# Optimization experiments

Measured on AMD Instinct MI355X. Metric: run time of the kernel, lower is better.

## Reference

```python
import jax, jax.numpy as jnp
import numpy as np

D_MODEL = 1024
HEADS = 16
D_K = 64
B, S = 2, 2048


def setup_inputs() -> dict:
    key = jax.random.key(0)
    ks = jax.random.split(key, 12)
    s = 0.02
    return {
        "query": jax.random.normal(ks[0], (B, S, D_MODEL), dtype=jnp.float32),
        "key": jax.random.normal(ks[1], (B, S, D_MODEL), dtype=jnp.float32),
        "value": jax.random.normal(ks[2], (B, S, D_MODEL), dtype=jnp.float32),
        "Wq": jax.random.normal(ks[3], (D_MODEL, HEADS * D_K), dtype=jnp.float32) * s,
        "bq": jnp.zeros((HEADS * D_K,), dtype=jnp.float32),
        "Wk": jax.random.normal(ks[4], (D_MODEL, HEADS * D_K), dtype=jnp.float32) * s,
        "bk": jnp.zeros((HEADS * D_K,), dtype=jnp.float32),
        "Wv": jax.random.normal(ks[5], (D_MODEL, HEADS * D_K), dtype=jnp.float32) * s,
        "bv": jnp.zeros((HEADS * D_K,), dtype=jnp.float32),
        "Wo": jax.random.normal(ks[6], (HEADS * D_K, D_MODEL), dtype=jnp.float32) * s,
        "bo": jnp.zeros((D_MODEL,), dtype=jnp.float32),
    }


def reference(query, key, value, Wq, bq, Wk, bk, Wv, bv, Wo, bo):
    b, s, _ = query.shape
    scale = 1.0 / np.sqrt(D_K).astype(np.float32)
    # project and split heads: [b, s, h, d_k]
    q = (query @ Wq + bq).reshape(b, s, HEADS, D_K)
    k = (key @ Wk + bk).reshape(b, s, HEADS, D_K)
    v = (value @ Wv + bv).reshape(b, s, HEADS, D_K)
    # attention scores [b, i, j, h]
    scores = jnp.einsum('bihd,bjhd->bijh', q, k) * scale
    # NOTE: original uses nn.Softmax(dim=1) -> normalize over query axis i (faithful quirk)
    attn = jax.nn.softmax(scores, axis=1)
    # dropout is identity in eval mode
    x = jnp.einsum('bijh,bjhd->bihd', attn, v).reshape(b, s, HEADS * D_K)
    return x @ Wo + bo
```

## Files before the change

### kernel.cpp

```cpp
#include <hip/hip_runtime.h>
#include <hip/hip_bf16.h>

#define SEQ   2048
#define NH    16
#define DK    64
#define DM    1024
#define NTOK  4096
#define C1    0.1803368801111204f

typedef unsigned short u16;
typedef unsigned int   u32;
typedef short bhalf8 __attribute__((ext_vector_type(8)));
typedef short bhalf4 __attribute__((ext_vector_type(4)));
typedef float floatx4 __attribute__((ext_vector_type(4)));

#define MFMA16(a,b,c) __builtin_amdgcn_mfma_f32_16x16x32_bf16(a,b,c,0,0,0)
#define MFMA4(a,b,c)  __builtin_amdgcn_mfma_f32_16x16x16bf16_1k(a,b,c,0,0,0)

#if __has_builtin(__builtin_amdgcn_exp2f)
#define EXP2(x) __builtin_amdgcn_exp2f(x)
#else
#define EXP2(x) exp2f(x)
#endif

__device__ __forceinline__ u16 f2b(float f){
  union { float f; u32 u; } v; v.f = f;
  u32 r = v.u + 0x7fffu + ((v.u >> 16) & 1u);
  return (u16)(r >> 16);
}
__device__ __forceinline__ u32 pk2(float a, float b){
  union { __hip_bfloat162 h; u32 w; } o;
  o.h = __float22bfloat162_rn(make_float2(a, b));
  return o.w;
}
__device__ __forceinline__ void gld_lds16(const u16* g, u16* lds){
  __builtin_amdgcn_global_load_lds(
      (const __attribute__((address_space(1))) u32*)g,
      (__attribute__((address_space(3))) u32*)lds, 16, 0, 0);
}

__global__ __launch_bounds__(256)
void cvt_qkv(const float* __restrict__ q, const float* __restrict__ k,
             const float* __restrict__ v, u16* __restrict__ Aq,
             u16* __restrict__ Ak, u16* __restrict__ Av)
{
  const float* in = (blockIdx.y == 0) ? q : (blockIdx.y == 1) ? k : v;
  u16* out       = (blockIdx.y == 0) ? Aq : (blockIdx.y == 1) ? Ak : Av;
  const size_t i = ((size_t)blockIdx.x * 256 + threadIdx.x) * 8;
  const float4 a = *(const float4*)(in + i);
  const float4 b = *(const float4*)(in + i + 4);
  uint4 o;
  o.x = pk2(a.x, a.y); o.y = pk2(a.z, a.w);
  o.z = pk2(b.x, b.y); o.w = pk2(b.z, b.w);
  *(uint4*)(out + i) = o;
}

__global__ __launch_bounds__(256)
void wtrans4(const float* __restrict__ Wq, const float* __restrict__ Wk,
             const float* __restrict__ Wv, const float* __restrict__ Wo,
             u16* __restrict__ Wtall)
{
  __shared__ __align__(16) u16 T[64][68];
  const int z = blockIdx.z;
  const float* W = (z == 0) ? Wq : (z == 1) ? Wk : (z == 2) ? Wv : Wo;
  u16* Wt = Wtall + (size_t)z * DM * DM;
  const int k0 = blockIdx.y * 64, n0 = blockIdx.x * 64;
  const int t = threadIdx.x;
  #pragma unroll
  for (int p = 0; p < 16; ++p){
    int e = p*256 + t, k = e >> 6, n = e & 63;
    T[n][k] = f2b(W[(size_t)(k0+k)*DM + n0 + n]);
  }
  __syncthreads();
  #pragma unroll
  for (int p = 0; p < 8; ++p){
    int e = p*256 + t, n = e >> 5, kp = e & 31;
    u32 val = *(const u32*)&T[n][2*kp];
    *(u32*)&Wt[(size_t)(n0+n)*DM + k0 + 2*kp] = val;
  }
}

__global__ __launch_bounds__(256)
void gemm_qkv(const u16* __restrict__ Aq, const u16* __restrict__ Ak,
              const u16* __restrict__ Av, const u16* __restrict__ Wtall,
              const float* __restrict__ bq, const float* __restrict__ bk,
              const float* __restrict__ bv, u16* __restrict__ Qb,
              u16* __restrict__ Kb, u16* __restrict__ Vt)
{
  __shared__ __align__(16) u16 Asm[2][128*32];
  __shared__ __align__(16) u16 Bsm[2][128*32];
  const int z = blockIdx.z;
  const u16* A = (z == 0) ? Aq : (z == 1) ? Ak : Av;
  const u16* Wt = Wtall + (size_t)z * DM * DM;
  const float* bias = (z == 0) ? bq : (z == 1) ? bk : bv;
  const float cmul = (z == 0) ? C1 : 1.0f;

  const int bm = blockIdx.y * 128, bn = blockIdx.x * 128;
  const int t = threadIdx.x, wid = t >> 6, l = t & 63, r16 = l & 15, q = l >> 4;
  const int wm = (wid & 1) * 64, wn = (wid >> 1) * 64;
  const int rL = t >> 2, gL = ((t & 3) ^ (rL & 3)) * 8;
  const u16* Ag = A  + (size_t)(bm + rL)*DM + gL;
  const u16* Bg = Wt + (size_t)(bn + rL)*DM + gL;
  const int wo = wid*512;
  const int sw = (r16 & 3);
  floatx4 acc[4][4] = {};

  gld_lds16(Ag,                  Asm[0] + wo);
  gld_lds16(Ag + (size_t)64*DM,  Asm[0] + wo + 2048);
  gld_lds16(Bg,                  Bsm[0] + wo);
  gld_lds16(Bg + (size_t)64*DM,  Bsm[0] + wo + 2048);
  __syncthreads();

  int cur = 0;
  for (int kc = 0; kc < DM; kc += 32){
    if (kc + 32 < DM){
      const int nx = cur ^ 1;
      gld_lds16(Ag + kc + 32,                 Asm[nx] + wo);
      gld_lds16(Ag + kc + 32 + (size_t)64*DM, Asm[nx] + wo + 2048);
      gld_lds16(Bg + kc + 32,                 Bsm[nx] + wo);
      gld_lds16(Bg + kc + 32 + (size_t)64*DM, Bsm[nx] + wo + 2048);
    }
    __builtin_amdgcn_s_setprio(1);
    bhalf8 af[4], bf[4];
    #pragma unroll
    for (int i = 0; i < 4; ++i)
      af[i] = *(const bhalf8*)&Asm[cur][(wm + i*16 + r16)*32 + ((q ^ sw)*8)];
    #pragma unroll
    for (int j = 0; j < 4; ++j)
      bf[j] = *(const bhalf8*)&Bsm[cur][(wn + j*16 + r16)*32 + ((q ^ sw)*8)];
    #pragma unroll
    for (int i = 0; i < 4; ++i)
      #pragma unroll
      for (int j = 0; j < 4; ++j)
        acc[i][j] = MFMA16(af[i], bf[j], acc[i][j]);
    __builtin_amdgcn_s_setprio(0);
    __syncthreads();
    cur ^= 1;
  }

  if (z < 2){
    u16* C = (z == 0) ? Qb : Kb;
    #pragma unroll
    for (int j = 0; j < 4; ++j){
      const int n = bn + wn + j*16 + r16;
      const float bj = bias[n];
      #pragma unroll
      for (int i = 0; i < 4; ++i){
        const int m0 = bm + wm + i*16 + q*4;
        #pragma unroll
        for (int r = 0; r < 4; ++r)
          C[(size_t)(m0+r)*DM + n] = f2b((acc[i][j][r] + bj) * cmul);
      }
    }
  } else {
    const int h  = (bn + wn) >> 6;
    const int bb = (bm + wm) >> 11;
    const int s0 = (bm + wm) & (SEQ - 1);
    #pragma unroll
    for (int i = 0; i < 4; ++i){
      const int sl = s0 + i*16 + q*4;
      #pragma unroll
      for (int j = 0; j < 4; ++j){
        const int d = j*16 + r16;
        const float bj = bias[h*DK + d];
        u32 v0 = pk2(acc[i][j][0]+bj, acc[i][j][1]+bj);
        u32 v1 = pk2(acc[i][j][2]+bj, acc[i][j][3]+bj);
        *(uint2*)&Vt[((size_t)(bb*NH + h)*DK + d)*SEQ + sl] = make_uint2(v0, v1);
      }
    }
  }
}

__global__ __launch_bounds__(256)
void gemm_o(const u16* __restrict__ A, const u16* __restrict__ Wt,
            const float* __restrict__ bias, float* __restrict__ C)
{
  __shared__ __align__(16) u16 Asm[2][128*32];
  __shared__ __align__(16) u16 Bsm[2][128*32];
  const int bm = blockIdx.y * 128, bn = blockIdx.x * 128;
  const int t = threadIdx.x, wid = t >> 6, l = t & 63, r16 = l & 15, q = l >> 4;
  const int wm = (wid & 1) * 64, wn = (wid >> 1) * 64;
  const int rL = t >> 2, gL = ((t & 3) ^ (rL & 3)) * 8;
  const u16* Ag = A  + (size_t)(bm + rL)*DM + gL;
  const u16* Bg = Wt + (size_t)(bn + rL)*DM + gL;
  const int wo = wid*512;
  const int sw = (r16 & 3);
  floatx4 acc[4][4] = {};

  gld_lds16(Ag,                  Asm[0] + wo);
  gld_lds16(Ag + (size_t)64*DM,  Asm[0] + wo + 2048);
  gld_lds16(Bg,                  Bsm[0] + wo);
  gld_lds16(Bg + (size_t)64*DM,  Bsm[0] + wo + 2048);
  __syncthreads();

  int cur = 0;
  for (int kc = 0; kc < DM; kc += 32){
    if (kc + 32 < DM){
      const int nx = cur ^ 1;
      gld_lds16(Ag + kc + 32,                 Asm[nx] + wo);
      gld_lds16(Ag + kc + 32 + (size_t)64*DM, Asm[nx] + wo + 2048);
      gld_lds16(Bg + kc + 32,                 Bsm[nx] + wo);
      gld_lds16(Bg + kc + 32 + (size_t)64*DM, Bsm[nx] + wo + 2048);
    }
    __builtin_amdgcn_s_setprio(1);
    bhalf8 af[4], bf[4];
    #pragma unroll
    for (int i = 0; i < 4; ++i)
      af[i] = *(const bhalf8*)&Asm[cur][(wm + i*16 + r16)*32 + ((q ^ sw)*8)];
    #pragma unroll
    for (int j = 0; j < 4; ++j)
      bf[j] = *(const bhalf8*)&Bsm[cur][(wn + j*16 + r16)*32 + ((q ^ sw)*8)];
    #pragma unroll
    for (int i = 0; i < 4; ++i)
      #pragma unroll
      for (int j = 0; j < 4; ++j)
        acc[i][j] = MFMA16(af[i], bf[j], acc[i][j]);
    __builtin_amdgcn_s_setprio(0);
    __syncthreads();
    cur ^= 1;
  }
  #pragma unroll
  for (int j = 0; j < 4; ++j){
    const int n = bn + wn + j*16 + r16;
    const float bj = bias[n];
    #pragma unroll
    for (int i = 0; i < 4; ++i){
      const int m0 = bm + wm + i*16 + q*4;
      #pragma unroll
      for (int r = 0; r < 4; ++r)
        C[(size_t)(m0+r)*DM + n] = acc[i][j][r] + bj;
    }
  }
}

__global__ __launch_bounds__(256)
void attn_stats(const u16* __restrict__ Qb, const u16* __restrict__ Kb,
                u16* __restrict__ Vt)
{
  __shared__ float pl[4][64];
  __shared__ float sLinv[64];
  const int j0 = blockIdx.x * 64, bh = blockIdx.y, b = bh >> 4, h = bh & 15;
  const int t = threadIdx.x, wid = t >> 6, l = t & 63, r16 = l & 15, q = l >> 4;

  bhalf8 kf[4][2];
  const u16* kp = Kb + (size_t)(b*SEQ + j0 + r16)*DM + h*DK + q*8;
  #pragma unroll
  for (int st = 0; st < 4; ++st){
    kf[st][0] = *(const bhalf8*)(kp + (size_t)st*16*DM);
    kf[st][1] = *(const bhalf8*)(kp + (size_t)st*16*DM + 32);
  }
  float rl[4] = {0.f, 0.f, 0.f, 0.f};
  const u16* qp = Qb + (size_t)(b*SEQ + wid*16 + r16)*DM + h*DK + q*8;
  for (int it = 0; it < SEQ/64; ++it){
    bhalf8 qf0 = *(const bhalf8*)qp;
    bhalf8 qf1 = *(const bhalf8*)(qp + 32);
    qp += (size_t)64*DM;
    #pragma unroll
    for (int st = 0; st < 4; ++st){
      floatx4 s = {};
      s = MFMA16(qf0, kf[st][0], s);
      s = MFMA16(qf1, kf[st][1], s);
      rl[st] += EXP2(s[0]) + EXP2(s[1]) + EXP2(s[2]) + EXP2(s[3]);
    }
  }
  #pragma unroll
  for (int st = 0; st < 4; ++st){
    float v = rl[st];
    v += __shfl_xor(v, 16);
    v += __shfl_xor(v, 32);
    rl[st] = v;
  }
  if (q == 0){
    #pragma unroll
    for (int st = 0; st < 4; ++st) pl[wid][st*16 + r16] = rl[st];
  }
  __syncthreads();
  if (t < 64)
    sLinv[t] = 1.f / (pl[0][t] + pl[1][t] + pl[2][t] + pl[3][t]);
  __syncthreads();
  {
    const int d = t >> 2, cb = (t & 3) * 16;
    u16* vp = Vt + ((size_t)bh*DK + d)*SEQ + j0 + cb;
    uint4 w0 = *(uint4*)vp, w1 = *(uint4*)(vp + 8);
    float sc[16];
    #pragma unroll
    for (int e = 0; e < 16; ++e) sc[e] = sLinv[cb + e];
    #define SC2(w, s0, s1) pk2(__uint_as_float((w) << 16) * (s0), \
                               __uint_as_float((w) & 0xffff0000u) * (s1))
    w0.x = SC2(w0.x, sc[0],  sc[1]);  w0.y = SC2(w0.y, sc[2],  sc[3]);
    w0.z = SC2(w0.z, sc[4],  sc[5]);  w0.w = SC2(w0.w, sc[6],  sc[7]);
    w1.x = SC2(w1.x, sc[8],  sc[9]);  w1.y = SC2(w1.y, sc[10], sc[11]);
    w1.z = SC2(w1.z, sc[12], sc[13]); w1.w = SC2(w1.w, sc[14], sc[15]);
    #undef SC2
    *(uint4*)vp = w0; *(uint4*)(vp + 8) = w1;
  }
}

__global__ __launch_bounds__(256)
void attn_pv(const u16* __restrict__ Qb, const u16* __restrict__ Kb,
             const u16* __restrict__ Vt, u16* __restrict__ Xb)
{
  __shared__ __align__(16) u16 Kls[2][64*64];
  __shared__ __align__(16) u16 Vls[2][64*64];
  const int i0 = blockIdx.x * 128, bh = blockIdx.y, b = bh >> 4, h = bh & 15;
  const int t = threadIdx.x, wid = t >> 6, l = t & 63, r16 = l & 15, q = l >> 4;

  bhalf8 qf[2][2];
  #pragma unroll
  for (int g = 0; g < 2; ++g){
    const u16* qp = Qb + (size_t)(b*SEQ + i0 + wid*32 + g*16 + r16)*DM + h*DK + q*8;
    qf[g][0] = *(const bhalf8*)qp;
    qf[g][1] = *(const bhalf8*)(qp + 32);
  }

  const int row0 = t >> 3, c0 = t & 7;
  const int g0 = (c0 ^ (row0 & 7)) * 8;
  const int row1 = row0 + 32;
  const int g1 = (c0 ^ (row1 & 7)) * 8;
  const u16* kp0 = Kb + (size_t)(b*SEQ + row0)*DM + h*DK + g0;
  const u16* kp1 = Kb + (size_t)(b*SEQ + row1)*DM + h*DK + g1;
  const u16* vp0 = Vt + ((size_t)bh*DK + row0)*SEQ + g0;
  const u16* vp1 = Vt + ((size_t)bh*DK + row1)*SEQ + g1;
  const int wo = wid*512;
  const int sw = (r16 & 7);

  floatx4 xaccT[2][4] = {};

  gld_lds16(kp0, &Kls[0][wo]);
  gld_lds16(kp1, &Kls[0][wo + 2048]);
  gld_lds16(vp0, &Vls[0][wo]);
  gld_lds16(vp1, &Vls[0][wo + 2048]);
  __syncthreads();

  int cur = 0;
  for (int jt = 0; jt < SEQ/64; ++jt){
    if (jt + 1 < SEQ/64){
      const int nx = cur ^ 1;
      gld_lds16(kp0 + (size_t)(jt+1)*64*DM, &Kls[nx][wo]);
      gld_lds16(kp1 + (size_t)(jt+1)*64*DM, &Kls[nx][wo + 2048]);
      gld_lds16(vp0 + (jt+1)*64,            &Vls[nx][wo]);
      gld_lds16(vp1 + (jt+1)*64,            &Vls[nx][wo + 2048]);
    }
    const u16* Kc = &Kls[cur][0];
    const u16* Vc = &Vls[cur][0];

    __builtin_amdgcn_s_setprio(1);
    bhalf4 pb[4][2];
    #pragma unroll
    for (int st = 0; st < 4; ++st){
      const int kr = (st*16 + r16) * 64;
      bhalf8 k0 = *(const bhalf8*)&Kc[kr + ((q     ^ sw) * 8)];
      bhalf8 k1 = *(const bhalf8*)&Kc[kr + (((q+4) ^ sw) * 8)];
      #pragma unroll
      for (int g = 0; g < 2; ++g){
        floatx4 s = {};
        s = MFMA16(k0, qf[g][0], s);
        s = MFMA16(k1, qf[g][1], s);
        union { uint2 u; bhalf4 h; } pu;
        pu.u = make_uint2(pk2(EXP2(s[0]), EXP2(s[1])),
                          pk2(EXP2(s[2]), EXP2(s[3])));
        pb[st][g] = pu.h;
      }
    }
    #pragma unroll
    for (int dst = 0; dst < 4; ++dst){
      bhalf4 va[4];
      #pragma unroll
      for (int st = 0; st < 4; ++st){
        const int ch = (st*2 + (q >> 1)) ^ (r16 & 7);
        va[st] = *(const bhalf4*)&Vc[(dst*16 + r16)*64 + ch*8 + (q & 1)*4];
      }
      #pragma unroll
      for (int g = 0; g < 2; ++g)
        #pragma unroll
        for (int st = 0; st < 4; ++st)
          xaccT[g][dst] = MFMA4(va[st], pb[st][g], xaccT[g][dst]);
    }
    __builtin_amdgcn_s_setprio(0);
    __syncthreads();
    cur ^= 1;
  }

  #pragma unroll
  for (int g = 0; g < 2; ++g){
    const size_t irow = (size_t)(b*SEQ + i0 + wid*32 + g*16 + r16);
    #pragma unroll
    for (int dst = 0; dst < 4; ++dst){
      u32 w0 = (u32)f2b(xaccT[g][dst][0]) | ((u32)f2b(xaccT[g][dst][1]) << 16);
      u32 w1 = (u32)f2b(xaccT[g][dst][2]) | ((u32)f2b(xaccT[g][dst][3]) << 16);
      *(uint2*)&Xb[irow*DM + h*DK + dst*16 + q*4] = make_uint2(w0, w1);
    }
  }
}

extern "C" void kernel_launch(void* const* d_in, const int* in_sizes, int n_in,
                              void* d_out, int out_size, void* d_ws, size_t ws_size,
                              hipStream_t stream)
{
  const float* q  = (const float*)d_in[0];
  const float* k  = (const float*)d_in[1];
  const float* v  = (const float*)d_in[2];
  const float* Wq = (const float*)d_in[3];
  const float* bq = (const float*)d_in[4];
  const float* Wk = (const float*)d_in[5];
  const float* bk = (const float*)d_in[6];
  const float* Wv = (const float*)d_in[7];
  const float* bv = (const float*)d_in[8];
  const float* Wo = (const float*)d_in[9];
  const float* bo = (const float*)d_in[10];
  float* out = (float*)d_out;

  char* ws = (char*)d_ws;
  const size_t WTB  = (size_t)DM * DM * sizeof(u16);
  const size_t TOKB = (size_t)NTOK * DM * sizeof(u16);
  u16* Wtall = (u16*)(ws);
  u16* Aq    = (u16*)(ws + 4*WTB);
  u16* Ak    = (u16*)(ws + 4*WTB + TOKB);
  u16* Av    = (u16*)(ws + 4*WTB + 2*TOKB);
  u16* Qb    = (u16*)(ws + 4*WTB + 3*TOKB);
  u16* Kb    = (u16*)(ws + 4*WTB + 4*TOKB);
  u16* Vt    = (u16*)(ws + 4*WTB + 5*TOKB);
  u16* Xb    = Aq;

  dim3 blk(256);
  cvt_qkv<<<dim3((NTOK*DM)/(256*8), 3), blk, 0, stream>>>(q, k, v, Aq, Ak, Av);
  wtrans4<<<dim3(16, 16, 4), blk, 0, stream>>>(Wq, Wk, Wv, Wo, Wtall);
  gemm_qkv<<<dim3(DM/128, NTOK/128, 3), blk, 0, stream>>>(
      Aq, Ak, Av, Wtall, bq, bk, bv, Qb, Kb, Vt);
  attn_stats<<<dim3(SEQ/64, NH*2), blk, 0, stream>>>(Qb, Kb, Vt);
  attn_pv<<<dim3(SEQ/128, NH*2), blk, 0, stream>>>(Qb, Kb, Vt, Xb);
  gemm_o<<<dim3(DM/128, NTOK/128), blk, 0, stream>>>(
      Xb, Wtall + 3*(size_t)DM*DM, bo, out);
}
```

Measured before the change: 269.0 us.

## Use 16x16x32 MFMA for PV product via permuted K row mapping

Replaces the 16x16x16 bf16 MFMAs in the P·V product with 16x16x32 MFMAs. K rows are reordered per lane so that two QK^T score tiles pack directly into a 32-wide bf16 P operand. The K LDS swizzle changes to match the new row access pattern, and V is now read as full 8-element vectors. This halves the PV MFMA instruction count and the number of V LDS reads, at the cost of a more complex row permutation and extra live score registers.

```diff
diff --git a/kernel.cpp b/kernel.cpp
--- a/kernel.cpp
+++ b/kernel.cpp
@@ -11,11 +11,9 @@
 typedef unsigned short u16;
 typedef unsigned int   u32;
 typedef short bhalf8 __attribute__((ext_vector_type(8)));
-typedef short bhalf4 __attribute__((ext_vector_type(4)));
 typedef float floatx4 __attribute__((ext_vector_type(4)));
 
 #define MFMA16(a,b,c) __builtin_amdgcn_mfma_f32_16x16x32_bf16(a,b,c,0,0,0)
-#define MFMA4(a,b,c)  __builtin_amdgcn_mfma_f32_16x16x16bf16_1k(a,b,c,0,0,0)
 
 #if __has_builtin(__builtin_amdgcn_exp2f)
 #define EXP2(x) __builtin_amdgcn_exp2f(x)
@@ -314,15 +312,19 @@
   }
 
   const int row0 = t >> 3, c0 = t & 7;
-  const int g0 = (c0 ^ (row0 & 7)) * 8;
+  const int fk0 = (row0 & 7) ^ (((row0 >> 3) & 1) << 2);
   const int row1 = row0 + 32;
-  const int g1 = (c0 ^ (row1 & 7)) * 8;
-  const u16* kp0 = Kb + (size_t)(b*SEQ + row0)*DM + h*DK + g0;
-  const u16* kp1 = Kb + (size_t)(b*SEQ + row1)*DM + h*DK + g1;
-  const u16* vp0 = Vt + ((size_t)bh*DK + row0)*SEQ + g0;
-  const u16* vp1 = Vt + ((size_t)bh*DK + row1)*SEQ + g1;
+  const int fk1 = (row1 & 7) ^ (((row1 >> 3) & 1) << 2);
+  const int gk0 = (c0 ^ fk0) * 8;
+  const int gk1 = (c0 ^ fk1) * 8;
+  const int gv0 = (c0 ^ (row0 & 7)) * 8;
+  const int gv1 = (c0 ^ (row1 & 7)) * 8;
+  const u16* kp0 = Kb + (size_t)(b*SEQ + row0)*DM + h*DK + gk0;
+  const u16* kp1 = Kb + (size_t)(b*SEQ + row1)*DM + h*DK + gk1;
+  const u16* vp0 = Vt + ((size_t)bh*DK + row0)*SEQ + gv0;
+  const u16* vp1 = Vt + ((size_t)bh*DK + row1)*SEQ + gv1;
   const int wo = wid*512;
-  const int sw = (r16 & 7);
+  const int swv = (r16 & 7);
 
   floatx4 xaccT[2][4] = {};
 
@@ -345,36 +347,43 @@
     const u16* Vc = &Vls[cur][0];
 
     __builtin_amdgcn_s_setprio(1);
-    bhalf4 pb[4][2];
-    #pragma unroll
-    for (int st = 0; st < 4; ++st){
-      const int kr = (st*16 + r16) * 64;
-      bhalf8 k0 = *(const bhalf8*)&Kc[kr + ((q     ^ sw) * 8)];
-      bhalf8 k1 = *(const bhalf8*)&Kc[kr + (((q+4) ^ sw) * 8)];
+    #pragma unroll
+    for (int h2 = 0; h2 < 2; ++h2){
+      floatx4 sacc[2][2];
+      #pragma unroll
+      for (int s = 0; s < 2; ++s){
+        const int jrow = h2*32 + (r16 >> 2)*8 + s*4 + (r16 & 3);
+        const int swr  = (jrow & 7) ^ (((jrow >> 3) & 1) << 2);
+        const int kr   = jrow * 64;
+        bhalf8 k0 = *(const bhalf8*)&Kc[kr + ((q     ^ swr) * 8)];
+        bhalf8 k1 = *(const bhalf8*)&Kc[kr + (((q+4) ^ swr) * 8)];
+        #pragma unroll
+        for (int g = 0; g < 2; ++g){
+          floatx4 s0 = {};
+          s0 = MFMA16(k0, qf[g][0], s0);
+          s0 = MFMA16(k1, qf[g][1], s0);
+          sacc[s][g] = s0;
+        }
+      }
+      bhalf8 pb[2];
       #pragma unroll
       for (int g = 0; g < 2; ++g){
-        floatx4 s = {};
-        s = MFMA16(k0, qf[g][0], s);
-        s = MFMA16(k1, qf[g][1], s);
-        union { uint2 u; bhalf4 h; } pu;
-        pu.u = make_uint2(pk2(EXP2(s[0]), EXP2(s[1])),
-                          pk2(EXP2(s[2]), EXP2(s[3])));
-        pb[st][g] = pu.h;
+        u32 w0 = pk2(EXP2(sacc[0][g][0]), EXP2(sacc[0][g][1]));
+        u32 w1 = pk2(EXP2(sacc[0][g][2]), EXP2(sacc[0][g][3]));
+        u32 w2 = pk2(EXP2(sacc[1][g][0]), EXP2(sacc[1][g][1]));
+        u32 w3 = pk2(EXP2(sacc[1][g][2]), EXP2(sacc[1][g][3]));
+        union { uint4 u; bhalf8 hh; } pu;
+        pu.u = make_uint4(w0, w1, w2, w3);
+        pb[g] = pu.hh;
       }
-    }
-    #pragma unroll
-    for (int dst = 0; dst < 4; ++dst){
-      bhalf4 va[4];
-      #pragma unroll
-      for (int st = 0; st < 4; ++st){
-        const int ch = (st*2 + (q >> 1)) ^ (r16 & 7);
-        va[st] = *(const bhalf4*)&Vc[(dst*16 + r16)*64 + ch*8 + (q & 1)*4];
+      #pragma unroll
+      for (int dst = 0; dst < 4; ++dst){
+        bhalf8 va = *(const bhalf8*)
+            &Vc[(dst*16 + r16)*64 + (((h2*4 + q) ^ swv) * 8)];
+        #pragma unroll
+        for (int g = 0; g < 2; ++g)
+          xaccT[g][dst] = MFMA16(va, pb[g], xaccT[g][dst]);
       }
-      #pragma unroll
-      for (int g = 0; g < 2; ++g)
-        #pragma unroll
-        for (int st = 0; st < 4; ++st)
-          xaccT[g][dst] = MFMA4(va[st], pb[st][g], xaccT[g][dst]);
     }
     __builtin_amdgcn_s_setprio(0);
     __syncthreads();
```

Result: faster. 263.3 us (-2.1%).
